# Optimization experiments

Hardware: AMD Instinct MI355X
Metric: run time of the kernel (lower is better)

## Reference

```python
import jax, jax.numpy as jnp
import numpy as np

N = 100000
E = 1000000
IN_C = 256
HID = 64
OUT = 64
NEG_SLOPE = 0.2


def setup_inputs() -> dict:
    key = jax.random.key(0)
    ks = jax.random.split(key, 12)
    x = jax.random.normal(ks[0], (N, IN_C), dtype=jnp.float32)
    edge_index = jax.random.randint(ks[1], (2, E), 0, N, dtype=jnp.int64)
    s = 1.0 / np.sqrt(IN_C)
    W1 = jax.random.uniform(ks[2], (IN_C, HID), jnp.float32, -s, s)
    a1_src = jax.random.uniform(ks[3], (HID,), jnp.float32, -s, s)
    a1_dst = jax.random.uniform(ks[4], (HID,), jnp.float32, -s, s)
    b1 = jnp.zeros((HID,), jnp.float32)
    s2 = 1.0 / np.sqrt(HID)
    W2 = jax.random.uniform(ks[5], (HID, OUT), jnp.float32, -s2, s2)
    a2_src = jax.random.uniform(ks[6], (OUT,), jnp.float32, -s2, s2)
    a2_dst = jax.random.uniform(ks[7], (OUT,), jnp.float32, -s2, s2)
    b2 = jnp.zeros((OUT,), jnp.float32)
    return {"x": x, "edge_index": edge_index, "W1": W1, "a1_src": a1_src,
            "a1_dst": a1_dst, "b1": b1, "W2": W2, "a2_src": a2_src,
            "a2_dst": a2_dst, "b2": b2}


def gat_conv(x, W, a_src, a_dst, b, src, dst):
    h = x @ W                              # [N, d]
    alpha_s = h @ a_src                    # [N]
    alpha_d = h @ a_dst                    # [N]
    e = jax.nn.leaky_relu(alpha_s[src] + alpha_d[dst], NEG_SLOPE)  # [E]
    # segment softmax over incoming edges of each destination node
    e_max = jax.lax.stop_gradient(jax.ops.segment_max(e, dst, num_segments=N))
    ex = jnp.exp(e - e_max[dst])
    denom = jax.ops.segment_sum(ex, dst, num_segments=N)
    alpha = ex / (denom[dst] + 1e-16)      # [E]
    out = jax.ops.segment_sum(alpha[:, None] * h[src], dst, num_segments=N)
    return out + b


def reference(x, edge_index, W1, a1_src, a1_dst, b1, W2, a2_src, a2_dst, b2):
    src, dst = edge_index[0], edge_index[1]
    # dropout(p=0.6) is identity in eval mode
    h = jax.nn.relu(gat_conv(x, W1, a1_src, a1_dst, b1, src, dst))
    out = gat_conv(h, W2, a2_src, a2_dst, b2, src, dst)
    return out
```

## Files before the change

kernel.cpp:

```cpp
#include <hip/hip_runtime.h>
#include <math.h>

#define HID 64
#define BSH 9
#define NPB 512
#define EPB 4096

typedef __attribute__((ext_vector_type(8))) short bf16x8;
typedef __attribute__((ext_vector_type(4))) float f32x4;
typedef __attribute__((ext_vector_type(4))) unsigned int u32x4;

__device__ __forceinline__ unsigned short f2bf(float f) {
    unsigned u = __float_as_uint(f);
    unsigned r = u + 0x7FFF + ((u >> 16) & 1);
    return (unsigned short)(r >> 16);
}
__device__ __forceinline__ float bf2f(unsigned short b) {
    return __uint_as_float(((unsigned)b) << 16);
}


__global__ __launch_bounds__(256) void bucket_count(const int* __restrict__ edst,
                                                    int* __restrict__ bcnt, int E_, int NB) {
    __shared__ int hist[256];
    int t = threadIdx.x;
    hist[t] = 0;
    __syncthreads();
    int base = blockIdx.x * EPB;
#pragma unroll
    for (int r = 0; r < EPB / 256; ++r) {
        int i = base + r * 256 + t;
        if (i < E_) atomicAdd(&hist[edst[i] >> BSH], 1);
    }
    __syncthreads();
    if (t < NB && hist[t]) atomicAdd(&bcnt[t], hist[t]);
}

__global__ __launch_bounds__(256) void scan_nb(const int* __restrict__ bcnt,
                                               int* __restrict__ bbase,
                                               int* __restrict__ bcur, int NB) {
    __shared__ int sd[256];
    int t = threadIdx.x;
    int v = (t < NB) ? bcnt[t] : 0;
    sd[t] = v;
    __syncthreads();
    for (int o = 1; o < 256; o <<= 1) {
        int u = (t >= o) ? sd[t - o] : 0;
        __syncthreads();
        sd[t] += u;
        __syncthreads();
    }
    int ex = sd[t] - v;
    if (t < NB) {
        bbase[t] = ex;
        bcur[t] = ex;
    }
    if (t == 0) bbase[NB] = sd[NB - 1];
}

__global__ __launch_bounds__(256) void bucket_scatter(const int* __restrict__ esrc,
                                                      const int* __restrict__ edst,
                                                      int* __restrict__ bcur,
                                                      int2* __restrict__ ebuf, int E_, int NB) {
    __shared__ int hist[256], chunk[256], lcur[256];
    int t = threadIdx.x;
    hist[t] = 0;
    lcur[t] = 0;
    __syncthreads();
    int base = blockIdx.x * EPB;
    int s[EPB / 256], d[EPB / 256];
#pragma unroll
    for (int r = 0; r < EPB / 256; ++r) {
        int i = base + r * 256 + t;
        if (i < E_) {
            s[r] = esrc[i];
            d[r] = edst[i];
            atomicAdd(&hist[d[r] >> BSH], 1);
        } else {
            d[r] = -1;
        }
    }
    __syncthreads();
    if (t < NB) chunk[t] = hist[t] ? atomicAdd(&bcur[t], hist[t]) : 0;
    __syncthreads();
#pragma unroll
    for (int r = 0; r < EPB / 256; ++r) {
        if (d[r] >= 0) {
            int b = d[r] >> BSH;
            int pos = chunk[b] + atomicAdd(&lcur[b], 1);
            ebuf[pos] = make_int2(s[r], d[r]);
        }
    }
}

__global__ __launch_bounds__(256) void csr_build(const int2* __restrict__ ebuf,
                                                 const int* __restrict__ bbase,
                                                 int* __restrict__ off,
                                                 int* __restrict__ srcs, int Nv, int NB) {
    __shared__ int dhist[NPB], dbase[NPB], psum[256];
    int b = blockIdx.x, t = threadIdx.x;
    int e0 = bbase[b], e1 = bbase[b + 1];
#pragma unroll
    for (int j = t; j < NPB; j += 256) dhist[j] = 0;
    __syncthreads();
    for (int i = e0 + t; i < e1; i += 256) {
        int d = ebuf[i].y;
        atomicAdd(&dhist[d & (NPB - 1)], 1);
    }
    __syncthreads();
    int a0 = dhist[2 * t], a1 = dhist[2 * t + 1];
    psum[t] = a0 + a1;
    __syncthreads();
    for (int o = 1; o < 256; o <<= 1) {
        int u = (t >= o) ? psum[t - o] : 0;
        __syncthreads();
        psum[t] += u;
        __syncthreads();
    }
    int ex = psum[t] - (a0 + a1);
    dbase[2 * t] = ex;
    dbase[2 * t + 1] = ex + a0;
    __syncthreads();
    for (int j = t; j < NPB; j += 256) {
        int node = (b << BSH) + j;
        if (node < Nv) off[node] = e0 + dbase[j];
    }
    if (b == NB - 1 && t == 0) off[Nv] = e1;
    __syncthreads();
    for (int i = e0 + t; i < e1; i += 256) {
        int2 p = ebuf[i];
        int pos = atomicAdd(&dbase[p.y & (NPB - 1)], 1);
        srcs[e0 + pos] = p.x;
    }
}


__global__ __launch_bounds__(256) void wt_kernel(const float* __restrict__ W,
                                                 unsigned short* __restrict__ Wt, int K) {
    int t = threadIdx.x;
    int k = blockIdx.x * 4 + (t >> 6);
    int n = t & 63;
    if (k < K) Wt[(size_t)n * K + k] = f2bf(W[(size_t)k * 64 + n]);
}


template <int K, bool BF16IN>
__global__ __launch_bounds__(256) void gemm_mfma(const void* __restrict__ Xv,
                                                 const unsigned short* __restrict__ Wt,
                                                 const float* __restrict__ a_s,
                                                 const float* __restrict__ a_d,
                                                 unsigned short* __restrict__ C,
                                                 float* __restrict__ as_,
                                                 float* __restrict__ ad_, int Nrows) {
    constexpr int KPAD = K + 8;
    constexpr int XPAD = 72;
    __shared__ __align__(16) unsigned short Ws[64 * KPAD];
    __shared__ __align__(16) unsigned short Xs[128 * XPAD];

    const float* Xf = (const float*)Xv;
    const unsigned short* Xb = (const unsigned short*)Xv;

    int t = threadIdx.x;
    int n0 = blockIdx.x * 128;
    int lane = t & 63;
    int w = t >> 6;
    int m = lane & 15;
    int q = lane >> 4;
    int base = n0 + w * 32;

    constexpr int KC8 = K / 8;
    for (int i = t; i < 64 * KC8; i += 256) {
        int n = i / KC8;
        int kc = i % KC8;
        u32x4 v = *(const u32x4*)(Wt + (size_t)n * K + kc * 8);
        *(u32x4*)(&Ws[n * KPAD + kc * 8]) = v;
    }

    f32x4 acc[2][4];
#pragma unroll
    for (int mi = 0; mi < 2; ++mi)
#pragma unroll
        for (int ct = 0; ct < 4; ++ct) acc[mi][ct] = (f32x4){0.f, 0.f, 0.f, 0.f};

    for (int k0 = 0; k0 < K; k0 += 64) {
        if (!BF16IN) {
#pragma unroll
            for (int i = 0; i < 8; ++i) {
                int idx = i * 256 + t;
                int row = idx >> 4;
                int kq = (idx & 15) * 4;
                int gn = n0 + row;
                if (gn >= Nrows) gn = Nrows - 1;
                float4 v = *(const float4*)(Xf + (size_t)gn * K + k0 + kq);
                ushort4 bb;
                bb.x = f2bf(v.x); bb.y = f2bf(v.y); bb.z = f2bf(v.z); bb.w = f2bf(v.w);
                *(ushort4*)(&Xs[row * XPAD + kq]) = bb;
            }
        } else {
#pragma unroll
            for (int i = 0; i < 4; ++i) {
                int idx = i * 256 + t;
                int row = idx >> 3;
                int kq = (idx & 7) * 8;
                int gn = n0 + row;
                if (gn >= Nrows) gn = Nrows - 1;
                u32x4 v = *(const u32x4*)(Xb + (size_t)gn * K + k0 + kq);
                *(u32x4*)(&Xs[row * XPAD + kq]) = v;
            }
        }
        __syncthreads();
#pragma unroll
        for (int ks = 0; ks < 64; ks += 32) {
            bf16x8 a0 = *(const bf16x8*)(&Xs[(w * 32 + m) * XPAD + ks + q * 8]);
            bf16x8 a1 = *(const bf16x8*)(&Xs[(w * 32 + 16 + m) * XPAD + ks + q * 8]);
#pragma unroll
            for (int ct = 0; ct < 4; ++ct) {
                bf16x8 bv = *(const bf16x8*)(&Ws[(ct * 16 + m) * KPAD + k0 + ks + q * 8]);
                acc[0][ct] = __builtin_amdgcn_mfma_f32_16x16x32_bf16(a0, bv, acc[0][ct], 0, 0, 0);
                acc[1][ct] = __builtin_amdgcn_mfma_f32_16x16x32_bf16(a1, bv, acc[1][ct], 0, 0, 0);
            }
        }
        __syncthreads();
    }

    float sa0 = a_s[m], sa1 = a_s[16 + m], sa2 = a_s[32 + m], sa3 = a_s[48 + m];
    float da0 = a_d[m], da1 = a_d[16 + m], da2 = a_d[32 + m], da3 = a_d[48 + m];

#pragma unroll
    for (int mi = 0; mi < 2; ++mi) {
#pragma unroll
        for (int r = 0; r < 4; ++r) {
            int row = base + mi * 16 + q * 4 + r;
            if (row < Nrows) {
                size_t ro = (size_t)row * 64 + m;
                C[ro]      = f2bf(acc[mi][0][r]);
                C[ro + 16] = f2bf(acc[mi][1][r]);
                C[ro + 32] = f2bf(acc[mi][2][r]);
                C[ro + 48] = f2bf(acc[mi][3][r]);
            }
        }
        float vs[4], vd[4];
#pragma unroll
        for (int r = 0; r < 4; ++r) {
            float s = acc[mi][0][r] * sa0 + acc[mi][1][r] * sa1 +
                      acc[mi][2][r] * sa2 + acc[mi][3][r] * sa3;
            float d = acc[mi][0][r] * da0 + acc[mi][1][r] * da1 +
                      acc[mi][2][r] * da2 + acc[mi][3][r] * da3;
#pragma unroll
            for (int o = 1; o < 16; o <<= 1) {
                s += __shfl_xor(s, o);
                d += __shfl_xor(d, o);
            }
            vs[r] = s;
            vd[r] = d;
        }
        if (m < 4) {
            int row = base + mi * 16 + q * 4 + m;
            float wvs = (m == 0) ? vs[0] : (m == 1) ? vs[1] : (m == 2) ? vs[2] : vs[3];
            float wvd = (m == 0) ? vd[0] : (m == 1) ? vd[1] : (m == 2) ? vd[2] : vd[3];
            if (row < Nrows) {
                as_[row] = wvs;
                ad_[row] = wvd;
            }
        }
    }
}


template <bool RELU_BF16OUT>
__global__ __launch_bounds__(256) void agg_kernel(const unsigned short* __restrict__ H,
                                                  const float* __restrict__ as_,
                                                  const float* __restrict__ ad_,
                                                  const float* __restrict__ bias,
                                                  const int* __restrict__ off,
                                                  const int* __restrict__ srcs,
                                                  void* __restrict__ outp, int Nrows) {
    int d = blockIdx.x * 4 + (threadIdx.x >> 6);
    int lane = threadIdx.x & 63;
    if (d >= Nrows) return;
    int begin = off[d], end = off[d + 1];
    float adv = ad_[d];
    float acc = 0.f, lsum = 0.f;

    for (int bbase = begin; bbase < end; bbase += 64) {
        int cnt = end - bbase;
        if (cnt > 64) cnt = 64;
        int s = 0;
        float p = 0.f;
        if (lane < cnt) {
            s = srcs[bbase + lane];
            float x = as_[s] + adv;
            x = (x > 0.f) ? x : 0.2f * x;
            p = __expf(x);
        }
        lsum += p;
        int nb = (cnt + 7) & ~7;
        for (int j = 0; j < nb; j += 8) {
            float hv[8], pv[8];
#pragma unroll
            for (int u = 0; u < 8; ++u) {
                int su = __builtin_amdgcn_readlane(s, j + u);
                pv[u] = __uint_as_float(
                    (unsigned)__builtin_amdgcn_readlane((int)__float_as_uint(p), j + u));
                hv[u] = bf2f(H[(size_t)su * HID + lane]);
            }
#pragma unroll
            for (int u = 0; u < 8; ++u) acc += pv[u] * hv[u];
        }
    }
#pragma unroll
    for (int o = 32; o; o >>= 1) lsum += __shfl_xor(lsum, o);
    float o = acc / (lsum + 1e-16f) + bias[lane];
    if (RELU_BF16OUT) {
        ((unsigned short*)outp)[(size_t)d * HID + lane] = f2bf(fmaxf(o, 0.f));
    } else {
        ((float*)outp)[(size_t)d * HID + lane] = o;
    }
}


extern "C" void kernel_launch(void* const* d_in, const int* in_sizes, int n_in,
                              void* d_out, int out_size, void* d_ws, size_t ws_size,
                              hipStream_t stream) {
    const float* x      = (const float*)d_in[0];
    const int*   edge   = (const int*)d_in[1];
    const float* W1     = (const float*)d_in[2];
    const float* a1_src = (const float*)d_in[3];
    const float* a1_dst = (const float*)d_in[4];
    const float* b1     = (const float*)d_in[5];
    const float* W2     = (const float*)d_in[6];
    const float* a2_src = (const float*)d_in[7];
    const float* a2_dst = (const float*)d_in[8];
    const float* b2     = (const float*)d_in[9];
    float* out = (float*)d_out;

    const int N = in_sizes[0] / 256;
    const int E = in_sizes[1] / 2;
    const int IN_C = 256;
    const int NB = (N + NPB - 1) >> BSH;

    char* w = (char*)d_ws;
    auto alloc = [&](size_t bytes) {
        char* p = w;
        w += (bytes + 255) & ~(size_t)255;
        return p;
    };
    int*            off   = (int*)alloc((size_t)(N + 1) * 4);
    int*            srcs  = (int*)alloc((size_t)E * 4);
    int2*           ebuf  = (int2*)alloc((size_t)E * 8);
    int*            bcnt  = (int*)alloc(256 * 4);
    int*            bbase = (int*)alloc(257 * 4);
    int*            bcur  = (int*)alloc(256 * 4);
    unsigned short* h1    = (unsigned short*)alloc((size_t)N * HID * 2);
    unsigned short* hB    = (unsigned short*)alloc((size_t)N * HID * 2);
    float*          as_   = (float*)alloc((size_t)N * 4);
    float*          ad_   = (float*)alloc((size_t)N * 4);
    unsigned short* Wt1   = (unsigned short*)alloc((size_t)IN_C * 64 * 2);
    unsigned short* Wt2   = (unsigned short*)alloc((size_t)64 * 64 * 2);

    const int* esrc = edge;
    const int* edst = edge + E;

    hipMemsetAsync(bcnt, 0, 256 * 4, stream);

    int gbk = (E + EPB - 1) / EPB;
    bucket_count<<<gbk, 256, 0, stream>>>(edst, bcnt, E, NB);
    scan_nb<<<1, 256, 0, stream>>>(bcnt, bbase, bcur, NB);
    bucket_scatter<<<gbk, 256, 0, stream>>>(esrc, edst, bcur, ebuf, E, NB);
    csr_build<<<NB, 256, 0, stream>>>(ebuf, bbase, off, srcs, N, NB);

    wt_kernel<<<IN_C / 4, 256, 0, stream>>>(W1, Wt1, IN_C);
    wt_kernel<<<64 / 4, 256, 0, stream>>>(W2, Wt2, 64);

    int gblocks = (N + 127) / 128;
    int ablocks = (N + 3) / 4;

    gemm_mfma<256, false><<<gblocks, 256, 0, stream>>>(x, Wt1, a1_src, a1_dst, h1, as_, ad_, N);
    agg_kernel<true><<<ablocks, 256, 0, stream>>>(h1, as_, ad_, b1, off, srcs, hB, N);

    gemm_mfma<64, true><<<gblocks, 256, 0, stream>>>(hB, Wt2, a2_src, a2_dst, h1, as_, ad_, N);
    agg_kernel<false><<<ablocks, 256, 0, stream>>>(h1, as_, ad_, b2, off, srcs, out, N);
}
```

Baseline: 329.3 us.

## Fuse preprocessing launches and vectorize aggregation with four edges per step

Merges bucket counting with both weight transposes into one launch, and merges the layer-1 GEMM with the edge bucket scatter into a heterogeneous grid so the independent CSR preprocessing overlaps the GEMM. The aggregation kernel now processes four edges at once, each 16-lane group loading four bf16 features with a vector load, then reduces across groups with shuffles. The aim is to cut launch overhead and idle tails and to widen memory accesses in the gather. The trade-off is dynamic shared memory sized for the GEMM on scatter blocks, and extra cross-lane shuffle reductions at the end of each node.

```diff
diff --git a/kernel.cpp b/kernel.cpp
--- a/kernel.cpp
+++ b/kernel.cpp
@@ -20,20 +20,36 @@
 }
 
 
-__global__ __launch_bounds__(256) void bucket_count(const int* __restrict__ edst,
-                                                    int* __restrict__ bcnt, int E_, int NB) {
+__global__ __launch_bounds__(256) void count_wt_kernel(const int* __restrict__ edst,
+                                                       int* __restrict__ bcnt, int E_, int NB,
+                                                       int gbk,
+                                                       const float* __restrict__ W1,
+                                                       unsigned short* __restrict__ Wt1, int K1,
+                                                       const float* __restrict__ W2,
+                                                       unsigned short* __restrict__ Wt2, int K2) {
     __shared__ int hist[256];
     int t = threadIdx.x;
-    hist[t] = 0;
-    __syncthreads();
-    int base = blockIdx.x * EPB;
-#pragma unroll
-    for (int r = 0; r < EPB / 256; ++r) {
-        int i = base + r * 256 + t;
-        if (i < E_) atomicAdd(&hist[edst[i] >> BSH], 1);
-    }
-    __syncthreads();
-    if (t < NB && hist[t]) atomicAdd(&bcnt[t], hist[t]);
+    int b = blockIdx.x;
+    if (b < gbk) {
+        hist[t] = 0;
+        __syncthreads();
+        int base = b * EPB;
+#pragma unroll
+        for (int r = 0; r < EPB / 256; ++r) {
+            int i = base + r * 256 + t;
+            if (i < E_) atomicAdd(&hist[edst[i] >> BSH], 1);
+        }
+        __syncthreads();
+        if (t < NB && hist[t]) atomicAdd(&bcnt[t], hist[t]);
+    } else if (b < gbk + 64) {
+        int k = (b - gbk) * 4 + (t >> 6);
+        int n = t & 63;
+        if (k < K1) Wt1[(size_t)n * K1 + k] = f2bf(W1[(size_t)k * 64 + n]);
+    } else {
+        int k = (b - gbk - 64) * 4 + (t >> 6);
+        int n = t & 63;
+        if (k < K2) Wt2[(size_t)n * K2 + k] = f2bf(W2[(size_t)k * 64 + n]);
+    }
 }
 
 __global__ __launch_bounds__(256) void scan_nb(const int* __restrict__ bcnt,
@@ -58,16 +74,17 @@
     if (t == 0) bbase[NB] = sd[NB - 1];
 }
 
-__global__ __launch_bounds__(256) void bucket_scatter(const int* __restrict__ esrc,
-                                                      const int* __restrict__ edst,
-                                                      int* __restrict__ bcur,
-                                                      int2* __restrict__ ebuf, int E_, int NB) {
-    __shared__ int hist[256], chunk[256], lcur[256];
+__device__ void scatter_body(char* smem, int b, const int* __restrict__ esrc,
+                             const int* __restrict__ edst, int* __restrict__ bcur,
+                             int2* __restrict__ ebuf, int E_, int NB) {
+    int* hist = (int*)smem;
+    int* chunk = hist + 256;
+    int* lcur = chunk + 256;
     int t = threadIdx.x;
     hist[t] = 0;
     lcur[t] = 0;
     __syncthreads();
-    int base = blockIdx.x * EPB;
+    int base = b * EPB;
     int s[EPB / 256], d[EPB / 256];
 #pragma unroll
     for (int r = 0; r < EPB / 256; ++r) {
@@ -86,8 +103,8 @@
 #pragma unroll
     for (int r = 0; r < EPB / 256; ++r) {
         if (d[r] >= 0) {
-            int b = d[r] >> BSH;
-            int pos = chunk[b] + atomicAdd(&lcur[b], 1);
+            int bk = d[r] >> BSH;
+            int pos = chunk[bk] + atomicAdd(&lcur[bk], 1);
             ebuf[pos] = make_int2(s[r], d[r]);
         }
     }
@@ -135,33 +152,22 @@
 }
 
 
-__global__ __launch_bounds__(256) void wt_kernel(const float* __restrict__ W,
-                                                 unsigned short* __restrict__ Wt, int K) {
-    int t = threadIdx.x;
-    int k = blockIdx.x * 4 + (t >> 6);
-    int n = t & 63;
-    if (k < K) Wt[(size_t)n * K + k] = f2bf(W[(size_t)k * 64 + n]);
-}
-
-
 template <int K, bool BF16IN>
-__global__ __launch_bounds__(256) void gemm_mfma(const void* __restrict__ Xv,
-                                                 const unsigned short* __restrict__ Wt,
-                                                 const float* __restrict__ a_s,
-                                                 const float* __restrict__ a_d,
-                                                 unsigned short* __restrict__ C,
-                                                 float* __restrict__ as_,
-                                                 float* __restrict__ ad_, int Nrows) {
+__device__ void gemm_body(char* smem, int bid, const void* __restrict__ Xv,
+                          const unsigned short* __restrict__ Wt,
+                          const float* __restrict__ a_s, const float* __restrict__ a_d,
+                          unsigned short* __restrict__ C, float* __restrict__ as_,
+                          float* __restrict__ ad_, int Nrows) {
     constexpr int KPAD = K + 8;
     constexpr int XPAD = 72;
-    __shared__ __align__(16) unsigned short Ws[64 * KPAD];
-    __shared__ __align__(16) unsigned short Xs[128 * XPAD];
+    unsigned short* Ws = (unsigned short*)smem;
+    unsigned short* Xs = (unsigned short*)(smem + (size_t)64 * KPAD * 2);
 
     const float* Xf = (const float*)Xv;
     const unsigned short* Xb = (const unsigned short*)Xv;
 
     int t = threadIdx.x;
-    int n0 = blockIdx.x * 128;
+    int n0 = bid * 128;
     int lane = t & 63;
     int w = t >> 6;
     int m = lane & 15;
@@ -264,6 +270,37 @@
             }
         }
     }
+}
+
+__global__ __launch_bounds__(256) void gemm1_scatter(const float* __restrict__ X,
+                                                     const unsigned short* __restrict__ Wt,
+                                                     const float* __restrict__ a_s,
+                                                     const float* __restrict__ a_d,
+                                                     unsigned short* __restrict__ C,
+                                                     float* __restrict__ as_,
+                                                     float* __restrict__ ad_, int Nrows,
+                                                     const int* __restrict__ esrc,
+                                                     const int* __restrict__ edst,
+                                                     int* __restrict__ bcur,
+                                                     int2* __restrict__ ebuf, int E_, int NB,
+                                                     int gblocks) {
+    extern __shared__ char smem[];
+    if ((int)blockIdx.x < gblocks) {
+        gemm_body<256, false>(smem, blockIdx.x, X, Wt, a_s, a_d, C, as_, ad_, Nrows);
+    } else {
+        scatter_body(smem, blockIdx.x - gblocks, esrc, edst, bcur, ebuf, E_, NB);
+    }
+}
+
+__global__ __launch_bounds__(256) void gemm2_kernel(const unsigned short* __restrict__ X,
+                                                    const unsigned short* __restrict__ Wt,
+                                                    const float* __restrict__ a_s,
+                                                    const float* __restrict__ a_d,
+                                                    unsigned short* __restrict__ C,
+                                                    float* __restrict__ as_,
+                                                    float* __restrict__ ad_, int Nrows) {
+    extern __shared__ char smem[];
+    gemm_body<64, true>(smem, blockIdx.x, X, Wt, a_s, a_d, C, as_, ad_, Nrows);
 }
 
 
@@ -280,7 +317,10 @@
     if (d >= Nrows) return;
     int begin = off[d], end = off[d + 1];
     float adv = ad_[d];
-    float acc = 0.f, lsum = 0.f;
+    int g = lane >> 4;
+    int c4 = (lane & 15) * 4;
+    float4 acc = {0.f, 0.f, 0.f, 0.f};
+    float lsum = 0.f;
 
     for (int bbase = begin; bbase < end; bbase += 64) {
         int cnt = end - bbase;
@@ -289,32 +329,48 @@
         float p = 0.f;
         if (lane < cnt) {
             s = srcs[bbase + lane];
-            float x = as_[s] + adv;
-            x = (x > 0.f) ? x : 0.2f * x;
-            p = __expf(x);
+            float xv = as_[s] + adv;
+            xv = (xv > 0.f) ? xv : 0.2f * xv;
+            p = __expf(xv);
         }
         lsum += p;
-        int nb = (cnt + 7) & ~7;
-        for (int j = 0; j < nb; j += 8) {
-            float hv[8], pv[8];
-#pragma unroll
-            for (int u = 0; u < 8; ++u) {
-                int su = __builtin_amdgcn_readlane(s, j + u);
-                pv[u] = __uint_as_float(
-                    (unsigned)__builtin_amdgcn_readlane((int)__float_as_uint(p), j + u));
-                hv[u] = bf2f(H[(size_t)su * HID + lane]);
-            }
-#pragma unroll
-            for (int u = 0; u < 8; ++u) acc += pv[u] * hv[u];
-        }
+        int nb = (cnt + 3) & ~3;
+        for (int j = 0; j < nb; j += 4) {
+            int sv = __shfl(s, j + g);
+            float pv = __shfl(p, j + g);
+            ushort4 hv = *(const ushort4*)(H + (size_t)sv * HID + c4);
+            acc.x += pv * bf2f(hv.x);
+            acc.y += pv * bf2f(hv.y);
+            acc.z += pv * bf2f(hv.z);
+            acc.w += pv * bf2f(hv.w);
+        }
+    }
+#pragma unroll
+    for (int o = 16; o <= 32; o <<= 1) {
+        acc.x += __shfl_xor(acc.x, o);
+        acc.y += __shfl_xor(acc.y, o);
+        acc.z += __shfl_xor(acc.z, o);
+        acc.w += __shfl_xor(acc.w, o);
     }
 #pragma unroll
     for (int o = 32; o; o >>= 1) lsum += __shfl_xor(lsum, o);
-    float o = acc / (lsum + 1e-16f) + bias[lane];
-    if (RELU_BF16OUT) {
-        ((unsigned short*)outp)[(size_t)d * HID + lane] = f2bf(fmaxf(o, 0.f));
-    } else {
-        ((float*)outp)[(size_t)d * HID + lane] = o;
+    if (g == 0) {
+        float inv = 1.f / (lsum + 1e-16f);
+        float4 b4 = *(const float4*)(bias + c4);
+        float o0 = acc.x * inv + b4.x;
+        float o1 = acc.y * inv + b4.y;
+        float o2 = acc.z * inv + b4.z;
+        float o3 = acc.w * inv + b4.w;
+        if (RELU_BF16OUT) {
+            ushort4 ov;
+            ov.x = f2bf(fmaxf(o0, 0.f));
+            ov.y = f2bf(fmaxf(o1, 0.f));
+            ov.z = f2bf(fmaxf(o2, 0.f));
+            ov.w = f2bf(fmaxf(o3, 0.f));
+            *(ushort4*)((unsigned short*)outp + (size_t)d * HID + c4) = ov;
+        } else {
+            *(float4*)((float*)outp + (size_t)d * HID + c4) = make_float4(o0, o1, o2, o3);
+        }
     }
 }
 
@@ -364,20 +420,19 @@
     hipMemsetAsync(bcnt, 0, 256 * 4, stream);
 
     int gbk = (E + EPB - 1) / EPB;
-    bucket_count<<<gbk, 256, 0, stream>>>(edst, bcnt, E, NB);
-    scan_nb<<<1, 256, 0, stream>>>(bcnt, bbase, bcur, NB);
-    bucket_scatter<<<gbk, 256, 0, stream>>>(esrc, edst, bcur, ebuf, E, NB);
-    csr_build<<<NB, 256, 0, stream>>>(ebuf, bbase, off, srcs, N, NB);
-
-    wt_kernel<<<IN_C / 4, 256, 0, stream>>>(W1, Wt1, IN_C);
-    wt_kernel<<<64 / 4, 256, 0, stream>>>(W2, Wt2, 64);
-
     int gblocks = (N + 127) / 128;
     int ablocks = (N + 3) / 4;
 
-    gemm_mfma<256, false><<<gblocks, 256, 0, stream>>>(x, Wt1, a1_src, a1_dst, h1, as_, ad_, N);
+    count_wt_kernel<<<gbk + 64 + 16, 256, 0, stream>>>(edst, bcnt, E, NB, gbk,
+                                                       W1, Wt1, IN_C, W2, Wt2, 64);
+    scan_nb<<<1, 256, 0, stream>>>(bcnt, bbase, bcur, NB);
+
+    size_t smem1 = (size_t)64 * (256 + 8) * 2 + (size_t)128 * 72 * 2;
+    gemm1_scatter<<<gblocks + gbk, 256, smem1, stream>>>(x, Wt1, a1_src, a1_dst, h1, as_, ad_, N,
+                                                         esrc, edst, bcur, ebuf, E, NB, gblocks);
+    csr_build<<<NB, 256, 0, stream>>>(ebuf, bbase, off, srcs, N, NB);
     agg_kernel<true><<<ablocks, 256, 0, stream>>>(h1, as_, ad_, b1, off, srcs, hB, N);
-
-    gemm_mfma<64, true><<<gblocks, 256, 0, stream>>>(hB, Wt2, a2_src, a2_dst, h1, as_, ad_, N);
+    size_t smem2 = (size_t)64 * (64 + 8) * 2 + (size_t)128 * 72 * 2;
+    gemm2_kernel<<<gblocks, 256, smem2, stream>>>(hB, Wt2, a2_src, a2_dst, h1, as_, ad_, N);
     agg_kernel<false><<<ablocks, 256, 0, stream>>>(h1, as_, ad_, b2, off, srcs, out, N);
 }
```

After: 332.3 us. No clear change (+0.9%).
